# Performance work log

Hardware: AMD Instinct MI355X
Metric: run time of the kernel (lower is better)

The kernel has to match this reference:

```python
import jax, jax.numpy as jnp
import numpy as np

B, S, D, H, L, DZ, POI, MAXP = 128, 512, 128, 4, 4, 128, 50000, 32
HD = D // H
EPS_LN = 1e-5

def layernorm(x, g, b):
    m = x.mean(-1, keepdims=True)
    v = ((x - m) ** 2).mean(-1, keepdims=True)
    return (x - m) * jax.lax.rsqrt(v + EPS_LN) * g + b

def setup_inputs() -> dict:
    key = jax.random.key(0)
    ks = iter(jax.random.split(key, 48))
    r = lambda shp, s=0.05: jax.random.normal(next(ks), shp, jnp.float32) * s
    return dict(
        d_t=jax.random.uniform(next(ks), (B, S), jnp.float32),
        d_l=jax.random.normal(next(ks), (B, S, 2), jnp.float32),
        d_emb=jax.random.randint(next(ks), (B, S), 0, POI),
        d_pad=jnp.zeros((B, S + 1), bool),
        num_pred=jax.random.randint(next(ks), (B,), 1, MAXP + 1),
        poi_table=r((POI, D), 0.02),
        W_time=r((D, 1)), W_space=r((D, 2)),
        agg_token=r((1, 1, D)),
        Wqkv=r((L, 3 * D, D), D ** -0.5), bqkv=jnp.zeros((L, 3 * D)),
        Wo=r((L, D, D), D ** -0.5), bo=jnp.zeros((L, D)),
        ln1_g=jnp.ones((L, D)), ln1_b=jnp.zeros((L, D)),
        W1=r((L, 2 * D, D), D ** -0.5), b1=jnp.zeros((L, 2 * D)),
        W2=r((L, D, 2 * D), (2 * D) ** -0.5), b2=jnp.zeros((L, D)),
        ln2_g=jnp.ones((L, D)), ln2_b=jnp.zeros((L, D)),
        Wg=r((DZ, D)), bg=jnp.zeros((DZ,)),
        Wt=r((DZ, D)), bt=jnp.zeros((DZ,)),
        gru_Wih=r((3 * D, D)), gru_Whh=r((3 * D, D)),
        gru_bih=jnp.zeros((3 * D,)), gru_bhh=jnp.zeros((3 * D,)),
        Wfc=r((1, D)), bfc=jnp.zeros((1,)),
    )

def reference(d_t, d_l, d_emb, d_pad, num_pred, poi_table, W_time, W_space, agg_token,
              Wqkv, bqkv, Wo, bo, ln1_g, ln1_b, W1, b1, W2, b2, ln2_g, ln2_b,
              Wg, bg, Wt, bt, gru_Wih, gru_Whh, gru_bih, gru_bhh, Wfc, bfc):
    # ---- Encoder: fused time/space/poi embeddings + agg token -> post-norm transformer stack ----
    t_emb = jnp.einsum('bs,d->bsd', d_t, W_time[:, 0])          # Linear(1, D, bias=False)
    c_emb = jnp.einsum('bsc,dc->bsd', d_l, W_space)             # Linear(2, D, bias=False)
    p_emb = poi_table[d_emb]                                    # [B,S,D]
    x = jnp.concatenate([t_emb + c_emb + p_emb,
                         jnp.broadcast_to(agg_token, (x_shape := (B, 1, D)))], axis=1)  # [B,S+1,D]
    T = S + 1
    neg = jnp.finfo(x.dtype).min
    for i in range(L):  # structurally distinct layers (post-norm, ReLU FFN, dropout=0)
        qkv = x @ Wqkv[i].T + bqkv[i]
        q, k, v = jnp.split(qkv, 3, axis=-1)
        hsplit = lambda t: t.reshape(B, T, H, HD).transpose(0, 2, 1, 3)
        q, k, v = hsplit(q), hsplit(k), hsplit(v)
        scores = jnp.einsum('bhqd,bhkd->bhqk', q, k) / jnp.sqrt(jnp.asarray(HD, x.dtype))
        scores = jnp.where(d_pad[:, None, None, :], neg, scores)
        attn = jax.nn.softmax(scores, axis=-1)
        o = jnp.einsum('bhqk,bhkd->bhqd', attn, v).transpose(0, 2, 1, 3).reshape(B, T, D)
        x = layernorm(x + o @ Wo[i].T + bo[i], ln1_g[i], ln1_b[i])
        ff = jax.nn.relu(x @ W1[i].T + b1[i]) @ W2[i].T + b2[i]
        x = layernorm(x + ff, ln2_g[i], ln2_b[i])
    ctx = x[:, -1, :]                                           # agg-token summary [B,D]
    gamma = ctx @ Wg.T + bg
    tau = jax.nn.softplus(ctx @ Wt.T + bt)

    # ---- DynamicTimeGenerator: batched GRUCell recurrence (input is the fixed zero init token) ----
    gi = jnp.zeros((1, D), ctx.dtype) @ gru_Wih.T + gru_bih      # [1,3D] input-side gates (x == 0)
    def step(h, _):
        gh = h @ gru_Whh.T + gru_bhh
        r = jax.nn.sigmoid(gi[:, :D] + gh[:, :D])
        z = jax.nn.sigmoid(gi[:, D:2 * D] + gh[:, D:2 * D])
        n = jnp.tanh(gi[:, 2 * D:] + r * gh[:, 2 * D:])
        h_new = (1.0 - z) * n + z * h
        delta = jax.nn.softplus(h_new @ Wfc.T + bfc)[:, 0]       # [B]
        return h_new, delta
    _, deltas = jax.lax.scan(step, ctx, None, length=MAXP)       # [MAXP, B]
    cum = jnp.cumsum(deltas, axis=0).T                           # [B, MAXP]
    last = jnp.take_along_axis(cum, (num_pred - 1)[:, None], axis=1)
    normed = cum / (last + 1e-6)
    valid = jnp.arange(MAXP)[None, :] < num_pred[:, None]
    times = jnp.zeros((B, MAXP + 2), ctx.dtype).at[:, 1:MAXP + 1].set(jnp.where(valid, normed, 0.0))
    times = times + jax.nn.one_hot(num_pred + 1, MAXP + 2, dtype=ctx.dtype)  # trailing 1.0 sentinel

    # ---- KL(q(z1)=N(gamma, tau^2) || N(0, I)) per kl_norm_norm ----
    a = jnp.sum(tau ** 2, -1, keepdims=True)
    b = jnp.sum(gamma ** 2, -1, keepdims=True)
    c = -2.0 * jnp.sum(jnp.log(tau), -1, keepdims=True)
    kl = 0.5 * (a + b + c - DZ)

    return jnp.concatenate([times, ctx, gamma, tau, kl], axis=-1)  # [B, MAXP+2+D+2*DZ+1]
```

## Files before the change

kernel.cpp:

```cpp
#include <hip/hip_runtime.h>

#define BB 128
#define SS 512
#define TT 513
#define DD 128
#define HH 4
#define LL 4
#define MM (BB*TT)

typedef __attribute__((ext_vector_type(4))) float f32x4;
typedef __attribute__((ext_vector_type(16))) float f32x16;
typedef __attribute__((ext_vector_type(8))) short short8;

typedef const __attribute__((address_space(1))) char* gas_t;
typedef __attribute__((address_space(3))) char* las_t;
#define GLDS16(g, l) __builtin_amdgcn_global_load_lds((gas_t)(g), (las_t)(l), 16, 0, 0)

__device__ __forceinline__ float b2f(ushort u){
  union { uint i; float f; } c; c.i = ((uint)u) << 16; return c.f;
}
__device__ __forceinline__ ushort f2b(float f){
  union { float f; uint i; } c; c.f = f;
  uint x = c.i;
  return (ushort)((x + 0x7fffu + ((x >> 16) & 1u)) >> 16);
}
union S8 { short8 v; ushort u[8]; };

__device__ __forceinline__ uint cvtpk(float lo, float hi){
  uint r;
  asm("v_cvt_pk_bf16_f32 %0, %1, %2" : "=v"(r) : "v"(lo), "v"(hi));
  return r;
}
__device__ __forceinline__ float fexp2(float x){
#if __has_builtin(__builtin_amdgcn_exp2f)
  return __builtin_amdgcn_exp2f(x);
#else
  return exp2f(x);
#endif
}

__global__ __launch_bounds__(256) void k_embed(
    const float* __restrict__ d_t, const float* __restrict__ d_l, const int* __restrict__ d_emb,
    const float* __restrict__ poi, const float* __restrict__ W_time, const float* __restrict__ W_space,
    const float* __restrict__ agg, ushort* __restrict__ xb)
{
  int gid = blockIdx.x*256 + threadIdx.x;
  if (gid >= MM*DD) return;
  int d = gid & 127;
  int m = gid >> 7;
  int b = m / TT, t = m % TT;
  float v;
  if (t == SS) v = agg[d];
  else {
    int bs = b*SS + t;
    v = d_t[bs]*W_time[d] + d_l[bs*2]*W_space[d*2] + d_l[bs*2+1]*W_space[d*2+1]
        + poi[(size_t)d_emb[bs]*DD + d];
  }
  xb[gid] = f2b(v);
}

__global__ __launch_bounds__(256) void k_f2b5(
    const float* __restrict__ s0, ushort* __restrict__ o0, int n0,
    const float* __restrict__ s1, ushort* __restrict__ o1, int n1,
    const float* __restrict__ s2, ushort* __restrict__ o2, int n2,
    const float* __restrict__ s3, ushort* __restrict__ o3, int n3,
    const float* __restrict__ s4, ushort* __restrict__ o4, int n4)
{
  int i = blockIdx.x*256 + threadIdx.x;
  if (i < n0){ o0[i] = f2b(s0[i]); return; } i -= n0;
  if (i < n1){ o1[i] = f2b(s1[i]); return; } i -= n1;
  if (i < n2){ o2[i] = f2b(s2[i]); return; } i -= n2;
  if (i < n3){ o3[i] = f2b(s3[i]); return; } i -= n3;
  if (i < n4){ o4[i] = f2b(s4[i]); }
}

template<bool RELU>
__global__ __launch_bounds__(512) void k_gemm2(
  const ushort* __restrict__ A, const ushort* __restrict__ W,
  const float* __restrict__ bias, ushort* __restrict__ Cout, const int N)
{
  __shared__ __align__(16) ushort As[128*128], Ws[64*128];
  const int tid = threadIdx.x;
  const int m0 = blockIdx.x * 128;
  const int l = tid & 63, wid = tid >> 6;
  const int wr = wid >> 1, wc = wid & 1;
  const int lr = l & 15, lg = l >> 4;
  #pragma unroll
  for (int i = tid; i < 2048; i += 512){
    const int row = i >> 4;
    const int ch  = (((i & 15)*16) ^ ((row & 7) << 4)) >> 4;
    GLDS16(&A[(size_t)(m0+row)*128 + ch*8], (char*)As + (size_t)(i - l)*16);
  }
  for (int n0 = 0; n0 < N; n0 += 64){
    if (n0) __syncthreads();
    #pragma unroll
    for (int i = tid; i < 1024; i += 512){
      const int row = i >> 4;
      const int ch  = (((i & 15)*16) ^ ((row & 7) << 4)) >> 4;
      GLDS16(&W[(size_t)(n0+row)*128 + ch*8], (char*)Ws + (size_t)(i - l)*16);
    }
    __syncthreads();
    f32x4 acc[2][2] = {};
    #pragma unroll
    for (int k0 = 0; k0 < 128; k0 += 32){
      const int sw = ((k0 + lg*8)*2) ^ ((lr & 7) << 4);
      short8 a0 = *(const short8*)((const char*)As + (wr*32+lr)*256 + sw);
      short8 a1 = *(const short8*)((const char*)As + (wr*32+16+lr)*256 + sw);
      short8 b0 = *(const short8*)((const char*)Ws + (wc*32+lr)*256 + sw);
      short8 b1 = *(const short8*)((const char*)Ws + (wc*32+16+lr)*256 + sw);
      acc[0][0] = __builtin_amdgcn_mfma_f32_16x16x32_bf16(a0, b0, acc[0][0], 0,0,0);
      acc[0][1] = __builtin_amdgcn_mfma_f32_16x16x32_bf16(a0, b1, acc[0][1], 0,0,0);
      acc[1][0] = __builtin_amdgcn_mfma_f32_16x16x32_bf16(a1, b0, acc[1][0], 0,0,0);
      acc[1][1] = __builtin_amdgcn_mfma_f32_16x16x32_bf16(a1, b1, acc[1][1], 0,0,0);
    }
    #pragma unroll
    for (int i=0;i<2;i++)
    #pragma unroll
    for (int j=0;j<2;j++)
    #pragma unroll
    for (int r=0;r<4;r++){
      const int lm = wr*32 + i*16 + lg*4 + r;
      const int ln = n0 + wc*32 + j*16 + lr;
      float v = acc[i][j][r] + bias[ln];
      if (RELU) v = fmaxf(v, 0.f);
      Cout[(size_t)(m0+lm)*N + ln] = f2b(v);
    }
  }
}

__global__ __launch_bounds__(512) void k_gemm_ln(
  const ushort* __restrict__ A, const ushort* __restrict__ W,
  const float* __restrict__ bias, ushort* __restrict__ xb,
  const float* __restrict__ g, const float* __restrict__ bb, const int K)
{
  __shared__ __align__(16) ushort As[128*128], Ws[128*128];
  const int tid = threadIdx.x;
  const int m0 = blockIdx.x * 128;
  const int l = tid & 63, w = tid >> 6;
  const int lr = l & 15, lg = l >> 4;
  f32x4 acc[8] = {};
  for (int kt = 0; kt < K; kt += 128){
    if (kt) __syncthreads();
    #pragma unroll
    for (int i = tid; i < 2048; i += 512){
      const int row = i >> 4;
      const int ch  = (((i & 15)*16) ^ ((row & 7) << 4)) >> 4;
      GLDS16(&A[(size_t)(m0+row)*K + kt + ch*8], (char*)As + (size_t)(i - l)*16);
    }
    #pragma unroll
    for (int i = tid; i < 2048; i += 512){
      const int row = i >> 4;
      const int ch  = (((i & 15)*16) ^ ((row & 7) << 4)) >> 4;
      GLDS16(&W[(size_t)row*K + kt + ch*8], (char*)Ws + (size_t)(i - l)*16);
    }
    __syncthreads();
    #pragma unroll
    for (int k0 = 0; k0 < 128; k0 += 32){
      const int sw = ((k0 + lg*8)*2) ^ ((lr & 7) << 4);
      short8 a = *(const short8*)((const char*)As + (w*16+lr)*256 + sw);
      #pragma unroll
      for (int j=0;j<8;j++){
        short8 bf = *(const short8*)((const char*)Ws + (j*16+lr)*256 + sw);
        acc[j] = __builtin_amdgcn_mfma_f32_16x16x32_bf16(a, bf, acc[j], 0,0,0);
      }
    }
  }
  float biasj[8], gj[8], bj[8];
  #pragma unroll
  for (int j=0;j<8;j++){ biasj[j]=bias[j*16+lr]; gj[j]=g[j*16+lr]; bj[j]=bb[j*16+lr]; }
  #pragma unroll
  for (int r=0;r<4;r++){
    const size_t row = (size_t)(m0 + w*16 + lg*4 + r);
    float resid[8], s=0.f, sq=0.f;
    #pragma unroll
    for (int j=0;j<8;j++){
      float v = acc[j][r] + biasj[j];
      resid[j] = b2f(xb[row*128 + j*16 + lr]) + v;
      s += resid[j]; sq += resid[j]*resid[j];
    }
    #pragma unroll
    for (int off=1; off<16; off<<=1){ s += __shfl_xor(s,off,64); sq += __shfl_xor(sq,off,64); }
    const float mean = s*(1.f/128.f);
    const float var  = fmaxf(sq*(1.f/128.f) - mean*mean, 0.f);
    const float rstd = rsqrtf(var + 1e-5f);
    #pragma unroll
    for (int j=0;j<8;j++){
      float o = (resid[j]-mean)*rstd*gj[j] + bj[j];
      xb[row*128 + j*16 + lr] = f2b(o);
    }
  }
}

#define VSTRIDE 544
#define NEGM 30000.f
#define MFMA32(a,b,c) __builtin_amdgcn_mfma_f32_32x32x16_bf16(a,b,c,0,0,0)

__global__ __launch_bounds__(512) void k_attn(const ushort* __restrict__ qkv, ushort* __restrict__ ao)
{
  __shared__ __align__(16) ushort KL[VSTRIDE*32];
  __shared__ __align__(16) ushort VT[32*VSTRIDE];
  const int tid = threadIdx.x;
  const int b = blockIdx.x >> 2, h = blockIdx.x & 3;
  const size_t base = (size_t)b*TT*384 + h*32;
  union { short4 v; ushort u[4]; } sv;
  for (int i = tid; i < 8*VSTRIDE; i += 512){
    int t = i >> 3, dc = (i & 7)*4;
    sv.u[0]=0; sv.u[1]=0; sv.u[2]=0; sv.u[3]=0;
    if (t < TT) sv.v = *(const short4*)&qkv[base + (size_t)t*384 + 128 + dc];
    *(short4*)((char*)KL + ((t*64 + dc*2) ^ ((t&7)<<4))) = sv.v;
  }
  for (int i = tid; i < 8*VSTRIDE; i += 512){
    int t = i >> 3, dc = (i & 7)*4;
    sv.u[0]=0; sv.u[1]=0; sv.u[2]=0; sv.u[3]=0;
    if (t < TT) sv.v = *(const short4*)&qkv[base + (size_t)t*384 + 256 + dc];
    #pragma unroll
    for (int e=0;e<4;e++){
      int d = dc + e;
      *(ushort*)((char*)VT + ((d*1088 + t*2) ^ ((d&7)<<4))) = sv.u[e];
    }
  }
  __syncthreads();
  const int l = tid & 63, w = tid >> 6;
  const int lq = l & 31, hi = l >> 5;
  const float qscale = 0.25503486341f;
  const int krow = (lq & 3) | ((lq & 4) << 1) | ((lq & 8) >> 1) | (lq & 16);
  f32x16 cinit;
  #pragma unroll
  for (int r=0;r<16;r++) cinit[r] = -40.f;

  for (int qi = 0; qi < 3; qi++){
    const int qb = w + qi*8;
    if (qb >= 17) break;
    const int q0 = qb*32;
    int qrow = q0 + lq; if (qrow > SS) qrow = SS;
    S8 qa, qf0, qf1;
    qa.v = *(const short8*)&qkv[base + (size_t)qrow*384 + hi*8];
    #pragma unroll
    for (int j=0;j<8;j++) qf0.u[j] = f2b(b2f(qa.u[j]) * qscale);
    qa.v = *(const short8*)&qkv[base + (size_t)qrow*384 + 16 + hi*8];
    #pragma unroll
    for (int j=0;j<8;j++) qf1.u[j] = f2b(b2f(qa.u[j]) * qscale);

    float rsl = 0.f;
    f32x16 acc = {};
    int t0 = 0;
    for (int kb = 0; kb < 17; kb++, t0 += 32){
      const int trow = t0 + krow;
      short8 kc0 = *(const short8*)((const char*)KL + ((trow*64 + hi*16)      ^ ((trow&7)<<4)));
      short8 kc1 = *(const short8*)((const char*)KL + ((trow*64 + 32 + hi*16) ^ ((trow&7)<<4)));
      f32x16 s = MFMA32(kc0, qf0.v, cinit);
      s = MFMA32(kc1, qf1.v, s);
      if (t0 + 32 > TT){
        #pragma unroll
        for (int r=0;r<16;r++){
          const int key = t0 + (r&7) + 8*hi + 16*(r>>3);
          if (key >= TT) s[r] = -NEGM;
        }
      }
      float p[16];
      #pragma unroll
      for (int r=0;r<16;r++){ p[r] = fexp2(s[r]); rsl += p[r]; }
      union { short8 v; uint u[4]; } pa0, pa1;
      #pragma unroll
      for (int wd=0; wd<4; wd++){
        pa0.u[wd] = cvtpk(p[2*wd],   p[2*wd+1]);
        pa1.u[wd] = cvtpk(p[8+2*wd], p[8+2*wd+1]);
      }
      short8 v0 = *(const short8*)((const char*)VT + (((lq*1088) + (t0 + hi*8)*2)      ^ ((lq&7)<<4)));
      short8 v1 = *(const short8*)((const char*)VT + (((lq*1088) + (t0 + 16 + hi*8)*2) ^ ((lq&7)<<4)));
      acc = MFMA32(v0, pa0.v, acc);
      acc = MFMA32(v1, pa1.v, acc);
    }
    rsl += __shfl_xor(rsl, 32, 64);
    if (q0 + lq < TT){
      const float inv = 1.f / rsl;
      ushort* orow = ao + ((size_t)(b*TT + q0 + lq))*DD + h*32;
      #pragma unroll
      for (int r=0;r<16;r++){
        const int d = (r&3) + 8*(r>>2) + 4*hi;
        orow[d] = f2b(acc[r]*inv);
      }
    }
  }
}

__global__ __launch_bounds__(256) void k_ctx(
    const ushort* __restrict__ xb, const float* __restrict__ Wg, const float* __restrict__ bg,
    const float* __restrict__ Wt, const float* __restrict__ bt,
    float* __restrict__ out, float* __restrict__ ctxws)
{
  __shared__ float cs[128];
  const int b = blockIdx.x, tid = threadIdx.x;
  const ushort* xr = &xb[((size_t)b*TT + SS)*128];
  if (tid < 128){
    float v = b2f(xr[tid]);
    cs[tid] = v;
    out[(size_t)b*419 + 34 + tid] = v;
    ctxws[b*128 + tid] = v;
  }
  __syncthreads();
  const int j = tid & 127;
  const float* Wrow = (tid < 128) ? &Wg[(size_t)j*128] : &Wt[(size_t)j*128];
  float acc = 0.f;
  #pragma unroll 8
  for (int d=0; d<128; d+=4){
    float4 wv = *(const float4*)&Wrow[d];
    acc += cs[d]*wv.x + cs[d+1]*wv.y + cs[d+2]*wv.z + cs[d+3]*wv.w;
  }
  if (tid < 128){
    out[(size_t)b*419 + 162 + j] = acc + bg[j];
  } else {
    float tv = acc + bt[j];
    float sp = fmaxf(tv, 0.f) + log1pf(__expf(-fabsf(tv)));
    out[(size_t)b*419 + 290 + j] = sp;
  }
}

#define GB 16
__global__ __launch_bounds__(512, 1) void k_gru(
    const float* __restrict__ ctx, const ushort* __restrict__ whh_b,
    const float* __restrict__ bih, const float* __restrict__ bhh,
    const float* __restrict__ Wfc, const float* __restrict__ bfc,
    float* __restrict__ deltas)
{
  __shared__ __align__(16) uint hb2[16*68];
  __shared__ __align__(16) float ghs[16*388];
  __shared__ float red[GB];
  const int tid = threadIdx.x;
  const int b0 = blockIdx.x * GB;
  const int l = tid & 63, w = tid >> 6;
  const int lr = l & 15, lg = l >> 4;
  short8 wb[3][4];
  #pragma unroll
  for (int t=0;t<3;t++){
    const int nrow = 16*w + t*128 + lr;
    #pragma unroll
    for (int kc=0;kc<4;kc++)
      wb[t][kc] = *(const short8*)&whh_b[(size_t)nrow*128 + kc*32 + lg*8];
  }
  const int ab = tid >> 5, ad = (tid & 31) * 4;
  float bi0a[4], bi1a[4], bi2a[4], bh0a[4], bh1a[4], bh2a[4], wfa[4];
  #pragma unroll
  for (int j=0;j<4;j++){
    bi0a[j]=bih[ad+j]; bi1a[j]=bih[128+ad+j]; bi2a[j]=bih[256+ad+j];
    bh0a[j]=bhh[ad+j]; bh1a[j]=bhh[128+ad+j]; bh2a[j]=bhh[256+ad+j];
    wfa[j]=Wfc[ad+j];
  }
  const float bfc0 = bfc[0];
  for (int i = tid; i < 16*64; i += 512){
    const int bb = i >> 6, j = i & 63;
    const float h0 = ctx[(size_t)(b0+bb)*128 + 2*j];
    const float h1 = ctx[(size_t)(b0+bb)*128 + 2*j + 1];
    hb2[bb*68 + j] = (uint)f2b(h0) | (((uint)f2b(h1)) << 16);
  }
  for (int step=0; step<32; step++){
    __syncthreads();
    if (step && tid < GB){
      const float dv = red[tid] + bfc0;
      deltas[(size_t)(b0+tid)*32 + (step-1)] = fmaxf(dv,0.f) + log1pf(__expf(-fabsf(dv)));
    }
    union { short8 v; uint4 q; } af[4];
    #pragma unroll
    for (int kc=0;kc<4;kc++)
      af[kc].q = *(const uint4*)&hb2[lr*68 + kc*16 + lg*4];
    f32x4 acc0 = {}, acc1 = {}, acc2 = {};
    #pragma unroll
    for (int kc=0;kc<4;kc++){
      acc0 = __builtin_amdgcn_mfma_f32_16x16x32_bf16(af[kc].v, wb[0][kc], acc0, 0,0,0);
      acc1 = __builtin_amdgcn_mfma_f32_16x16x32_bf16(af[kc].v, wb[1][kc], acc1, 0,0,0);
      acc2 = __builtin_amdgcn_mfma_f32_16x16x32_bf16(af[kc].v, wb[2][kc], acc2, 0,0,0);
    }
    #pragma unroll
    for (int r=0;r<4;r++){
      ghs[(lg*4+r)*388 + 16*w + lr]       = acc0[r];
      ghs[(lg*4+r)*388 + 16*w + 128 + lr] = acc1[r];
      ghs[(lg*4+r)*388 + 16*w + 256 + lr] = acc2[r];
    }
    __syncthreads();
    float4 gr = *(const float4*)&ghs[ab*388 + ad];
    float4 gz = *(const float4*)&ghs[ab*388 + 128 + ad];
    float4 gn = *(const float4*)&ghs[ab*388 + 256 + ad];
    const float grs[4] = {gr.x,gr.y,gr.z,gr.w};
    const float gzs[4] = {gz.x,gz.y,gz.z,gz.w};
    const float gns[4] = {gn.x,gn.y,gn.z,gn.w};
    const uint hp0 = hb2[ab*68 + (ad>>1)], hp1 = hb2[ab*68 + (ad>>1) + 1];
    const float h[4] = { b2f((ushort)hp0), b2f((ushort)(hp0>>16)),
                         b2f((ushort)hp1), b2f((ushort)(hp1>>16)) };
    float hn[4], pv = 0.f;
    #pragma unroll
    for (int j=0;j<4;j++){
      const float rr = 1.f/(1.f + __expf(-(bi0a[j] + bh0a[j] + grs[j])));
      const float zz = 1.f/(1.f + __expf(-(bi1a[j] + bh1a[j] + gzs[j])));
      const float nn = tanhf(bi2a[j] + rr*(gns[j] + bh2a[j]));
      hn[j] = (1.f - zz)*nn + zz*h[j];
      pv += hn[j]*wfa[j];
    }
    hb2[ab*68 + (ad>>1)]     = (uint)f2b(hn[0]) | (((uint)f2b(hn[1])) << 16);
    hb2[ab*68 + (ad>>1) + 1] = (uint)f2b(hn[2]) | (((uint)f2b(hn[3])) << 16);
    #pragma unroll
    for (int off=1; off<32; off<<=1) pv += __shfl_xor(pv, off, 64);
    if ((tid & 31) == 0) red[ab] = pv;
  }
  __syncthreads();
  if (tid < GB){
    const float dv = red[tid] + bfc0;
    deltas[(size_t)(b0+tid)*32 + 31] = fmaxf(dv,0.f) + log1pf(__expf(-fabsf(dv)));
  }
}

__global__ __launch_bounds__(64) void k_final(
    const float* __restrict__ deltas, const int* __restrict__ num_pred,
    float* __restrict__ out)
{
  const int b = blockIdx.x, l = threadIdx.x;
  float d = (l < 32) ? deltas[b*32 + l] : 0.f;
  float c = d;
  #pragma unroll
  for (int off=1; off<32; off<<=1){
    float t = __shfl_up(c, off, 64);
    if (l >= off) c += t;
  }
  const int np = num_pred[b];
  float last = __shfl(c, np-1, 64);
  float denom = last + 1e-6f;
  float cjm = __shfl(c, (l==0 ? 0 : l-1), 64);
  float val = 0.f;
  if (l >= 1 && l <= 32 && (l-1) < np) val = cjm / denom;
  if (l == np + 1) val += 1.f;
  if (l < 34) out[(size_t)b*419 + l] = val;
  float ta = 0.f, tb = 0.f, tc = 0.f;
  for (int z = l; z < 128; z += 64){
    float ga = out[(size_t)b*419 + 162 + z];
    float tu = fmaxf(out[(size_t)b*419 + 290 + z], 1e-35f);
    ta += tu*tu; tb += ga*ga; tc += -2.f*logf(tu);
  }
  float v = ta + tb + tc;
  #pragma unroll
  for (int off=1; off<64; off<<=1) v += __shfl_xor(v, off, 64);
  if (l == 0) out[(size_t)b*419 + 418] = 0.5f*(v - 128.f);
}

extern "C" void kernel_launch(void* const* d_in, const int* in_sizes, int n_in,
                              void* d_out, int out_size, void* d_ws, size_t ws_size,
                              hipStream_t stream)
{
  (void)in_sizes; (void)n_in; (void)out_size; (void)ws_size;
  const float* d_t    = (const float*)d_in[0];
  const float* d_l    = (const float*)d_in[1];
  const int*   d_emb  = (const int*)  d_in[2];
  const int*   numprd = (const int*)  d_in[4];
  const float* poi    = (const float*)d_in[5];
  const float* W_time = (const float*)d_in[6];
  const float* W_space= (const float*)d_in[7];
  const float* agg    = (const float*)d_in[8];
  const float* Wqkv   = (const float*)d_in[9];
  const float* bqkv   = (const float*)d_in[10];
  const float* Wo     = (const float*)d_in[11];
  const float* bo     = (const float*)d_in[12];
  const float* ln1g   = (const float*)d_in[13];
  const float* ln1b   = (const float*)d_in[14];
  const float* W1     = (const float*)d_in[15];
  const float* b1     = (const float*)d_in[16];
  const float* W2     = (const float*)d_in[17];
  const float* b2     = (const float*)d_in[18];
  const float* ln2g   = (const float*)d_in[19];
  const float* ln2b   = (const float*)d_in[20];
  const float* Wg     = (const float*)d_in[21];
  const float* bg     = (const float*)d_in[22];
  const float* Wt     = (const float*)d_in[23];
  const float* bt     = (const float*)d_in[24];
  const float* Whh    = (const float*)d_in[26];
  const float* bih    = (const float*)d_in[27];
  const float* bhh    = (const float*)d_in[28];
  const float* Wfc    = (const float*)d_in[29];
  const float* bfc    = (const float*)d_in[30];
  float* out = (float*)d_out;

  char* ws = (char*)d_ws;
  size_t off = 0;
  auto alloc = [&](size_t bytes){ size_t o = off; off += (bytes + 255) & ~(size_t)255; return o; };
  ushort* xb    = (ushort*)(ws + alloc((size_t)MM*128*2));
  ushort* qkv   = (ushort*)(ws + alloc((size_t)MM*384*2));
  ushort* aob   = (ushort*)(ws + alloc((size_t)MM*128*2));
  ushort* hb    = (ushort*)(ws + alloc((size_t)MM*256*2));
  ushort* wqkvb = (ushort*)(ws + alloc((size_t)LL*384*128*2));
  ushort* wob   = (ushort*)(ws + alloc((size_t)LL*128*128*2));
  ushort* w1b   = (ushort*)(ws + alloc((size_t)LL*256*128*2));
  ushort* w2b   = (ushort*)(ws + alloc((size_t)LL*128*256*2));
  ushort* whhb  = (ushort*)(ws + alloc((size_t)384*128*2));
  float*  ctxws = (float*) (ws + alloc(128*128*4));
  float*  deltas= (float*) (ws + alloc(128*32*4));

  const int n0 = LL*384*128, n1 = LL*128*128, n2 = LL*256*128, n3 = LL*128*256, n4 = 384*128;
  k_f2b5<<<(n0+n1+n2+n3+n4+255)/256,256,0,stream>>>(Wqkv,wqkvb,n0, Wo,wob,n1, W1,w1b,n2, W2,w2b,n3, Whh,whhb,n4);
  k_embed<<<(MM*DD)/256,256,0,stream>>>(d_t, d_l, d_emb, poi, W_time, W_space, agg, xb);

  for (int li = 0; li < LL; li++){
    k_gemm2<false><<<MM/128,512,0,stream>>>(xb, wqkvb + li*384*128, bqkv + li*384, qkv, 384);
    k_attn<<<BB*HH,512,0,stream>>>(qkv, aob);
    k_gemm_ln<<<MM/128,512,0,stream>>>(aob, wob + li*128*128, bo + li*128, xb,
                                       ln1g + li*128, ln1b + li*128, 128);
    k_gemm2<true><<<MM/128,512,0,stream>>>(xb, w1b + li*256*128, b1 + li*256, hb, 256);
    k_gemm_ln<<<MM/128,512,0,stream>>>(hb, w2b + li*128*256, b2 + li*128, xb,
                                       ln2g + li*128, ln2b + li*128, 256);
  }

  k_ctx<<<128,256,0,stream>>>(xb, Wg, bg, Wt, bt, out, ctxws);
  k_gru<<<8,512,0,stream>>>(ctxws, whhb, bih, bhh, Wfc, bfc, deltas);
  k_final<<<128,64,0,stream>>>(deltas, numprd, out);
}
```

Measured before the change: 498.2 us.

## Fuse FFN up-projection, ReLU, down-projection and LayerNorm into one kernel

New measurement: 480.4 us, median of 2. 1.04x faster.

```diff
diff --git a/kernel.cpp b/kernel.cpp
--- a/kernel.cpp
+++ b/kernel.cpp
@@ -186,6 +186,103 @@
     #pragma unroll
     for (int j=0;j<8;j++){
       float o = (resid[j]-mean)*rstd*gj[j] + bj[j];
+      xb[row*128 + j*16 + lr] = f2b(o);
+    }
+  }
+}
+
+__global__ __launch_bounds__(512) void k_ffn(
+  const ushort* __restrict__ A, const ushort* __restrict__ W1, const float* __restrict__ b1,
+  const ushort* __restrict__ W2, const float* __restrict__ b2,
+  ushort* __restrict__ xb, const float* __restrict__ g, const float* __restrict__ bb)
+{
+  __shared__ __align__(16) ushort As[128*128];
+  __shared__ __align__(16) ushort W1s[64*128];
+  __shared__ __align__(16) ushort W2s[128*64];
+  __shared__ __align__(16) ushort Hs[128*64];
+  const int tid = threadIdx.x;
+  const int m0 = blockIdx.x * 128;
+  const int l = tid & 63, w = tid >> 6;
+  const int lr = l & 15, lg = l >> 4;
+  #pragma unroll
+  for (int i = tid; i < 2048; i += 512){
+    const int row = i >> 4;
+    const int ch  = (((i & 15)*16) ^ ((row & 7) << 4)) >> 4;
+    GLDS16(&A[(size_t)(m0+row)*128 + ch*8], (char*)As + (size_t)(i - l)*16);
+  }
+  f32x4 acc2[8] = {};
+  for (int c = 0; c < 4; c++){
+    __syncthreads();
+    #pragma unroll
+    for (int i = tid; i < 1024; i += 512){
+      const int row = i >> 4;
+      const int ch  = (((i & 15)*16) ^ ((row & 7) << 4)) >> 4;
+      GLDS16(&W1[(size_t)(c*64+row)*128 + ch*8], (char*)W1s + (size_t)(i - l)*16);
+    }
+    #pragma unroll
+    for (int i = tid; i < 1024; i += 512){
+      const int row = i >> 3;
+      const int ch  = (i & 7) ^ (row & 7);
+      GLDS16(&W2[(size_t)row*256 + c*64 + ch*8], (char*)W2s + (size_t)(i - l)*16);
+    }
+    __syncthreads();
+    f32x4 acc1[4] = {};
+    #pragma unroll
+    for (int k0 = 0; k0 < 128; k0 += 32){
+      const int sw = ((k0 + lg*8)*2) ^ ((lr & 7) << 4);
+      short8 a = *(const short8*)((const char*)As + (w*16+lr)*256 + sw);
+      #pragma unroll
+      for (int j=0;j<4;j++){
+        short8 bf = *(const short8*)((const char*)W1s + (j*16+lr)*256 + sw);
+        acc1[j] = __builtin_amdgcn_mfma_f32_16x16x32_bf16(a, bf, acc1[j], 0,0,0);
+      }
+    }
+    #pragma unroll
+    for (int j=0;j<4;j++){
+      const float b1j = b1[c*64 + j*16 + lr];
+      #pragma unroll
+      for (int r=0;r<4;r++){
+        const int row = w*16 + lg*4 + r;
+        const int col = j*16 + lr;
+        const float v = fmaxf(acc1[j][r] + b1j, 0.f);
+        *(ushort*)((char*)Hs + ((row*128 + col*2) ^ ((row & 7) << 4))) = f2b(v);
+      }
+    }
+    __syncthreads();
+    #pragma unroll
+    for (int kk=0; kk<2; kk++){
+      const int sw2 = (kk*32 + lg*8)*2;
+      short8 ha = *(const short8*)((const char*)Hs + (((w*16+lr)*128 + sw2) ^ ((lr & 7) << 4)));
+      #pragma unroll
+      for (int j=0;j<8;j++){
+        short8 wf = *(const short8*)((const char*)W2s + (((j*16+lr)*128 + sw2) ^ ((lr & 7) << 4)));
+        acc2[j] = __builtin_amdgcn_mfma_f32_16x16x32_bf16(ha, wf, acc2[j], 0,0,0);
+      }
+    }
+  }
+  float biasj[8], gj[8], bj[8];
+  #pragma unroll
+  for (int j=0;j<8;j++){ biasj[j]=b2[j*16+lr]; gj[j]=g[j*16+lr]; bj[j]=bb[j*16+lr]; }
+  #pragma unroll
+  for (int r=0;r<4;r++){
+    const int rl = w*16 + lg*4 + r;
+    const size_t row = (size_t)(m0 + rl);
+    float resid[8], s=0.f, sq=0.f;
+    #pragma unroll
+    for (int j=0;j<8;j++){
+      const float v = acc2[j][r] + biasj[j];
+      const ushort xu = *(const ushort*)((const char*)As + ((rl*256 + (j*16+lr)*2) ^ ((rl & 7) << 4)));
+      resid[j] = b2f(xu) + v;
+      s += resid[j]; sq += resid[j]*resid[j];
+    }
+    #pragma unroll
+    for (int off=1; off<16; off<<=1){ s += __shfl_xor(s,off,64); sq += __shfl_xor(sq,off,64); }
+    const float mean = s*(1.f/128.f);
+    const float var  = fmaxf(sq*(1.f/128.f) - mean*mean, 0.f);
+    const float rstd = rsqrtf(var + 1e-5f);
+    #pragma unroll
+    for (int j=0;j<8;j++){
+      const float o = (resid[j]-mean)*rstd*gj[j] + bj[j];
       xb[row*128 + j*16 + lr] = f2b(o);
     }
   }
@@ -482,7 +579,6 @@
   ushort* xb    = (ushort*)(ws + alloc((size_t)MM*128*2));
   ushort* qkv   = (ushort*)(ws + alloc((size_t)MM*384*2));
   ushort* aob   = (ushort*)(ws + alloc((size_t)MM*128*2));
-  ushort* hb    = (ushort*)(ws + alloc((size_t)MM*256*2));
   ushort* wqkvb = (ushort*)(ws + alloc((size_t)LL*384*128*2));
   ushort* wob   = (ushort*)(ws + alloc((size_t)LL*128*128*2));
   ushort* w1b   = (ushort*)(ws + alloc((size_t)LL*256*128*2));
@@ -500,9 +596,9 @@
     k_attn<<<BB*HH,512,0,stream>>>(qkv, aob);
     k_gemm_ln<<<MM/128,512,0,stream>>>(aob, wob + li*128*128, bo + li*128, xb,
                                        ln1g + li*128, ln1b + li*128, 128);
-    k_gemm2<true><<<MM/128,512,0,stream>>>(xb, w1b + li*256*128, b1 + li*256, hb, 256);
-    k_gemm_ln<<<MM/128,512,0,stream>>>(hb, w2b + li*128*256, b2 + li*128, xb,
-                                       ln2g + li*128, ln2b + li*128, 256);
+    k_ffn<<<MM/128,512,0,stream>>>(xb, w1b + li*256*128, b1 + li*256,
+                                   w2b + li*128*256, b2 + li*128, xb,
+                                   ln2g + li*128, ln2b + li*128);
   }
 
   k_ctx<<<128,256,0,stream>>>(xb, Wg, bg, Wt, bt, out, ctxws);
```
